# Kernel tuning notes

Measured on AMD Instinct MI355X. Metric: run time of the kernel, lower is better.

The kernel has to match this reference:

```python
import jax, jax.numpy as jnp
import numpy as np

COUT, CIN = 1024, 1024  # self.shape = (cout, cin) in the torch module
NNZ = 131072


def setup_inputs() -> dict:
    key = jax.random.key(0)
    k_x, k_v, k_r, k_c = jax.random.split(key, 4)
    x = jax.random.normal(k_x, (4, 4096, CIN), dtype=jnp.float32)
    values = jax.random.normal(k_v, (NNZ,), dtype=jnp.float32)
    rows = jax.random.randint(k_r, (NNZ,), 0, COUT, dtype=jnp.int32)
    cols = jax.random.randint(k_c, (NNZ,), 0, CIN, dtype=jnp.int32)
    indices = jnp.stack([rows, cols], axis=0)  # [2, nnz], integer-valued
    return {"x": x, "values": values, "indices": indices}


def reference(x, values, indices):
    # torch: sparse_coo_tensor(indices, values, (cout, cin)).coalesce();
    # coalescing sums duplicate (row, col) entries -> scatter-add densify.
    rows, cols = indices[0], indices[1]
    W = jnp.zeros((COUT, CIN), dtype=values.dtype).at[rows, cols].add(values)
    # 3D path: out[b, l, co] = sum_ci W[co, ci] * x[b, l, ci]
    return jnp.einsum('blc,oc->blo', x, W)
```

## Files before the change

kernel.cpp:

```cpp
#include <hip/hip_runtime.h>
#include <cstdint>
#include <cstddef>

#define CIN  1024
#define COUT 1024

__device__ __forceinline__ unsigned short f2bf(float f) {
    union { float f; unsigned int i; } v;
    v.f = f;
    unsigned int u = v.i;
    u += 0x7FFFu + ((u >> 16) & 1u);
    return (unsigned short)(u >> 16);
}

__global__ void zero_f32(float4* __restrict__ p) {
    p[blockIdx.x * 256 + threadIdx.x] = float4{0.f, 0.f, 0.f, 0.f};
}

__global__ void scatter_add(const float* __restrict__ vals,
                            const int* __restrict__ rows,
                            const int* __restrict__ cols,
                            float* __restrict__ W, int nnz) {
    int i = blockIdx.x * 256 + threadIdx.x;
    if (i < nnz) {
        atomicAdd(W + (size_t)rows[i] * CIN + cols[i], vals[i]);
    }
}

__global__ void cvt_bf16(const float* __restrict__ src, unsigned short* __restrict__ dst) {
    int i = (blockIdx.x * 256 + threadIdx.x) * 4;
    float4 v = *(const float4*)(src + i);
    ushort4 o;
    o.x = f2bf(v.x); o.y = f2bf(v.y); o.z = f2bf(v.z); o.w = f2bf(v.w);
    *(ushort4*)(dst + i) = o;
}

typedef __attribute__((ext_vector_type(8))) short bf16x8;
typedef __attribute__((ext_vector_type(4))) float f32x4;

__global__ __launch_bounds__(256) void gemm_af32_bbf16(
    const float* __restrict__ A,
    const unsigned short* __restrict__ B,
    float* __restrict__ C,
    int M) {
    constexpr int K = CIN;
    constexpr int N = COUT;

    __shared__ __align__(16) unsigned short As[128 * 64];
    __shared__ __align__(16) unsigned short Bs[128 * 64];

    const int tid   = threadIdx.x;
    const int lane  = tid & 63;
    const int wave  = tid >> 6;
    const int waveM = (wave >> 1) * 64;
    const int waveN = (wave & 1) * 64;
    const int quad  = lane >> 4;
    const int l16   = lane & 15;

    const int rowA0 = blockIdx.x * 128;
    const int rowB0 = blockIdx.y * 128;

    const int stg_m = tid >> 3;
    const int stg_k = (tid & 7) * 8;
    const float*          pa = A + (size_t)(rowA0 + stg_m) * K + stg_k;
    const unsigned short* pb = B + (size_t)(rowB0 + stg_m) * K + stg_k;
    const int ldsoff = tid * 8;

    f32x4 acc[4][4] = {};

    for (int k0 = 0; k0 < K; k0 += 64) {
#pragma unroll
        for (int it = 0; it < 4; ++it) {
            __builtin_amdgcn_global_load_lds(
                (const __attribute__((address_space(1))) void*)(pb + k0 + (size_t)it * 32 * K),
                (__attribute__((address_space(3))) void*)(Bs + it * 2048 + ldsoff),
                16, 0, 0);
        }
#pragma unroll
        for (int it = 0; it < 4; ++it) {
            const float* s = pa + k0 + (size_t)it * 32 * K;
            float4 v0 = *(const float4*)(s);
            float4 v1 = *(const float4*)(s + 4);
            union { bf16x8 v; unsigned short u[8]; } w;
            w.u[0] = f2bf(v0.x); w.u[1] = f2bf(v0.y);
            w.u[2] = f2bf(v0.z); w.u[3] = f2bf(v0.w);
            w.u[4] = f2bf(v1.x); w.u[5] = f2bf(v1.y);
            w.u[6] = f2bf(v1.z); w.u[7] = f2bf(v1.w);
            *(bf16x8*)(As + it * 2048 + ldsoff) = w.v;
        }
        __syncthreads();

#pragma unroll
        for (int ks = 0; ks < 2; ++ks) {
            bf16x8 af[4], bfr[4];
#pragma unroll
            for (int t = 0; t < 4; ++t) {
                af[t]  = *(const bf16x8*)(As + (waveM + t * 16 + l16) * 64 + ks * 32 + quad * 8);
                bfr[t] = *(const bf16x8*)(Bs + (waveN + t * 16 + l16) * 64 + ks * 32 + quad * 8);
            }
#pragma unroll
            for (int i = 0; i < 4; ++i)
#pragma unroll
                for (int j = 0; j < 4; ++j)
                    acc[i][j] = __builtin_amdgcn_mfma_f32_16x16x32_bf16(
                        af[i], bfr[j], acc[i][j], 0, 0, 0);
        }
        __syncthreads();
    }

#pragma unroll
    for (int i = 0; i < 4; ++i) {
#pragma unroll
        for (int r = 0; r < 4; ++r) {
            const int row = rowA0 + waveM + i * 16 + quad * 4 + r;
            float* cp = C + (size_t)row * N + rowB0 + waveN + l16;
#pragma unroll
            for (int j = 0; j < 4; ++j)
                cp[j * 16] = acc[i][j][r];
        }
    }
}

extern "C" void kernel_launch(void* const* d_in, const int* in_sizes, int n_in,
                              void* d_out, int out_size, void* d_ws, size_t ws_size,
                              hipStream_t stream) {
    const float* x    = (const float*)d_in[0];
    const float* vals = (const float*)d_in[1];
    const int*   idx  = (const int*)d_in[2];

    float* out = (float*)d_out;

    const int nnz = in_sizes[2] / 2;
    const int M   = in_sizes[0] / CIN;

    float*          Wf = (float*)d_ws;
    unsigned short* Wb = (unsigned short*)((char*)d_ws + (size_t)COUT * CIN * sizeof(float));

    zero_f32<<<dim3(COUT * CIN / (256 * 4)), dim3(256), 0, stream>>>((float4*)Wf);
    scatter_add<<<dim3((nnz + 255) / 256), dim3(256), 0, stream>>>(vals, idx, idx + nnz, Wf, nnz);
    cvt_bf16<<<dim3(COUT * CIN / (256 * 4)), dim3(256), 0, stream>>>(Wf, Wb);
    gemm_af32_bbf16<<<dim3(M / 128, COUT / 128), dim3(256), 0, stream>>>(x, Wb, out, M);
}
```

Before: 180.3 us.

## Pre-convert activations to bf16 and swizzle LDS tiles in GEMM

Adds a separate bulk pass that converts x to bf16 into workspace, so the GEMM can stage both A and B tiles with direct global-to-LDS loads instead of loading fp32 into registers and converting per tile. It also applies an XOR swizzle to the LDS column layout to reduce bank conflicts on the fragment reads. The cost is an extra kernel that reads x in fp32 and writes a bf16 copy (about 96 MB of traffic for M=16384), plus more workspace. In return the GEMM reads half as many A bytes and drops the conversion ALU work from its inner loop.

```diff
diff --git a/kernel.cpp b/kernel.cpp
--- a/kernel.cpp
+++ b/kernel.cpp
@@ -4,6 +4,9 @@
 
 #define CIN  1024
 #define COUT 1024
+
+typedef __attribute__((ext_vector_type(8))) short bf16x8;
+typedef __attribute__((ext_vector_type(4))) float f32x4;
 
 __device__ __forceinline__ unsigned short f2bf(float f) {
     union { float f; unsigned int i; } v;
@@ -27,19 +30,18 @@
     }
 }
 
-__global__ void cvt_bf16(const float* __restrict__ src, unsigned short* __restrict__ dst) {
-    int i = (blockIdx.x * 256 + threadIdx.x) * 4;
-    float4 v = *(const float4*)(src + i);
-    ushort4 o;
-    o.x = f2bf(v.x); o.y = f2bf(v.y); o.z = f2bf(v.z); o.w = f2bf(v.w);
-    *(ushort4*)(dst + i) = o;
+__global__ void cvt_bf16_bulk(const float* __restrict__ src, unsigned short* __restrict__ dst) {
+    size_t i = ((size_t)blockIdx.x * 256 + threadIdx.x) * 8;
+    float4 v0 = *(const float4*)(src + i);
+    float4 v1 = *(const float4*)(src + i + 4);
+    union { bf16x8 v; unsigned short u[8]; } w;
+    w.u[0] = f2bf(v0.x); w.u[1] = f2bf(v0.y); w.u[2] = f2bf(v0.z); w.u[3] = f2bf(v0.w);
+    w.u[4] = f2bf(v1.x); w.u[5] = f2bf(v1.y); w.u[6] = f2bf(v1.z); w.u[7] = f2bf(v1.w);
+    *(bf16x8*)(dst + i) = w.v;
 }
 
-typedef __attribute__((ext_vector_type(8))) short bf16x8;
-typedef __attribute__((ext_vector_type(4))) float f32x4;
-
-__global__ __launch_bounds__(256) void gemm_af32_bbf16(
-    const float* __restrict__ A,
+__global__ __launch_bounds__(256) void gemm_bt_bf16_sw(
+    const unsigned short* __restrict__ A,
     const unsigned short* __restrict__ B,
     float* __restrict__ C,
     int M) {
@@ -60,10 +62,11 @@
     const int rowA0 = blockIdx.x * 128;
     const int rowB0 = blockIdx.y * 128;
 
-    const int stg_m = tid >> 3;
-    const int stg_k = (tid & 7) * 8;
-    const float*          pa = A + (size_t)(rowA0 + stg_m) * K + stg_k;
-    const unsigned short* pb = B + (size_t)(rowB0 + stg_m) * K + stg_k;
+    const int stg_r  = tid >> 3;
+    const int c_slot = tid & 7;
+    const int c_data = c_slot ^ (stg_r & 7);
+    const unsigned short* pa = A + (size_t)(rowA0 + stg_r) * K + c_data * 8;
+    const unsigned short* pb = B + (size_t)(rowB0 + stg_r) * K + c_data * 8;
     const int ldsoff = tid * 8;
 
     f32x4 acc[4][4] = {};
@@ -72,31 +75,25 @@
 #pragma unroll
         for (int it = 0; it < 4; ++it) {
             __builtin_amdgcn_global_load_lds(
+                (const __attribute__((address_space(1))) void*)(pa + k0 + (size_t)it * 32 * K),
+                (__attribute__((address_space(3))) void*)(As + it * 2048 + ldsoff),
+                16, 0, 0);
+            __builtin_amdgcn_global_load_lds(
                 (const __attribute__((address_space(1))) void*)(pb + k0 + (size_t)it * 32 * K),
                 (__attribute__((address_space(3))) void*)(Bs + it * 2048 + ldsoff),
                 16, 0, 0);
         }
-#pragma unroll
-        for (int it = 0; it < 4; ++it) {
-            const float* s = pa + k0 + (size_t)it * 32 * K;
-            float4 v0 = *(const float4*)(s);
-            float4 v1 = *(const float4*)(s + 4);
-            union { bf16x8 v; unsigned short u[8]; } w;
-            w.u[0] = f2bf(v0.x); w.u[1] = f2bf(v0.y);
-            w.u[2] = f2bf(v0.z); w.u[3] = f2bf(v0.w);
-            w.u[4] = f2bf(v1.x); w.u[5] = f2bf(v1.y);
-            w.u[6] = f2bf(v1.z); w.u[7] = f2bf(v1.w);
-            *(bf16x8*)(As + it * 2048 + ldsoff) = w.v;
-        }
         __syncthreads();
 
+        const int s7 = l16 & 7;
 #pragma unroll
         for (int ks = 0; ks < 2; ++ks) {
             bf16x8 af[4], bfr[4];
+            const int cx = ((ks * 4 + quad) ^ s7) * 8;
 #pragma unroll
             for (int t = 0; t < 4; ++t) {
-                af[t]  = *(const bf16x8*)(As + (waveM + t * 16 + l16) * 64 + ks * 32 + quad * 8);
-                bfr[t] = *(const bf16x8*)(Bs + (waveN + t * 16 + l16) * 64 + ks * 32 + quad * 8);
+                af[t]  = *(const bf16x8*)(As + (waveM + t * 16 + l16) * 64 + cx);
+                bfr[t] = *(const bf16x8*)(Bs + (waveN + t * 16 + l16) * 64 + cx);
             }
 #pragma unroll
             for (int i = 0; i < 4; ++i)
@@ -133,11 +130,16 @@
     const int nnz = in_sizes[2] / 2;
     const int M   = in_sizes[0] / CIN;
 
+    const size_t wf_bytes = (size_t)COUT * CIN * sizeof(float);
+    const size_t wb_bytes = (size_t)COUT * CIN * sizeof(unsigned short);
+
     float*          Wf = (float*)d_ws;
-    unsigned short* Wb = (unsigned short*)((char*)d_ws + (size_t)COUT * CIN * sizeof(float));
+    unsigned short* Wb = (unsigned short*)((char*)d_ws + wf_bytes);
+    unsigned short* Xb = (unsigned short*)((char*)d_ws + wf_bytes + wb_bytes);
 
     zero_f32<<<dim3(COUT * CIN / (256 * 4)), dim3(256), 0, stream>>>((float4*)Wf);
     scatter_add<<<dim3((nnz + 255) / 256), dim3(256), 0, stream>>>(vals, idx, idx + nnz, Wf, nnz);
-    cvt_bf16<<<dim3(COUT * CIN / (256 * 4)), dim3(256), 0, stream>>>(Wf, Wb);
-    gemm_af32_bbf16<<<dim3(M / 128, COUT / 128), dim3(256), 0, stream>>>(x, Wb, out, M);
+    cvt_bf16_bulk<<<dim3(COUT * CIN / (256 * 8)), dim3(256), 0, stream>>>(Wf, Wb);
+    cvt_bf16_bulk<<<dim3((unsigned)((size_t)M * CIN / (256 * 8))), dim3(256), 0, stream>>>(x, Xb);
+    gemm_bt_bf16_sw<<<dim3(M / 128, COUT / 128), dim3(256), 0, stream>>>(Xb, Wb, out, M);
 }
```

Result: faster. 163.8 us (-9.1%).
